# Performance work log

Hardware: AMD Instinct MI355X
Metric: run time of the kernel (lower is better)

The kernel has to match this reference:

```python
import jax, jax.numpy as jnp
import numpy as np

H = W = 32      # latent grid
WS = 8          # window size
NH = 8          # heads
C = 512         # channels
SHIFTS = (0, WS // 2)  # depth-2 Swin stage: W-MSA then SW-MSA


def _rel_pos_index(ws):
    coords = np.stack(np.meshgrid(np.arange(ws), np.arange(ws), indexing='ij'))
    flat = coords.reshape(2, -1)
    rel = (flat[:, :, None] - flat[:, None, :]).transpose(1, 2, 0).copy()
    rel[:, :, 0] += ws - 1
    rel[:, :, 1] += ws - 1
    rel[:, :, 0] *= 2 * ws - 1
    return jnp.asarray(rel.sum(-1))  # (ws*ws, ws*ws) int


def _attn_mask(h, w, ws, shift):
    img = np.zeros((h, w))
    cnt = 0
    sl = (slice(0, -ws), slice(-ws, -shift), slice(-shift, None))
    for hs in sl:
        for wsl in sl:
            img[hs, wsl] = cnt
            cnt += 1
    mw = img.reshape(h // ws, ws, w // ws, ws).transpose(0, 2, 1, 3).reshape(-1, ws * ws)
    m = mw[:, None, :] - mw[:, :, None]  # matches unsqueeze(1) - unsqueeze(2)
    return jnp.asarray(np.where(m != 0, -100.0, 0.0).astype(np.float32))  # (nW, N, N)


def _ln(x, g, b, eps=1e-5):
    mu = x.mean(-1, keepdims=True)
    var = ((x - mu) ** 2).mean(-1, keepdims=True)
    return (x - mu) * jax.lax.rsqrt(var + eps) * g + b


def _swin_block(x, shift, mask, rpi, n1g, n1b, qw, qb, rpb, pw, pb, n2g, n2b, f1w, f1b, f2w, f2b):
    B, L, Cc = x.shape
    N = WS * WS
    hd = Cc // NH
    shortcut = x
    h = _ln(x, n1g, n1b).reshape(B, H, W, Cc)
    if shift > 0:
        h = jnp.roll(h, (-shift, -shift), (1, 2))
    # window partition -> (B*nW, N, C)
    hw = h.reshape(B, H // WS, WS, W // WS, WS, Cc).transpose(0, 1, 3, 2, 4, 5).reshape(-1, N, Cc)
    qkv = (hw @ qw + qb).reshape(-1, N, 3, NH, hd).transpose(2, 0, 3, 1, 4)
    q, k, v = qkv[0], qkv[1], qkv[2]
    attn = jnp.einsum('bhnd,bhmd->bhnm', q * (hd ** -0.5), k)
    bias = rpb[rpi.reshape(-1)].reshape(N, N, NH).transpose(2, 0, 1)  # (NH, N, N)
    attn = attn + bias[None]
    if mask is not None:
        nW = mask.shape[0]
        attn = attn.reshape(-1, nW, NH, N, N) + mask[None, :, None]
        attn = attn.reshape(-1, NH, N, N)
    attn = jax.nn.softmax(attn, axis=-1)
    o = jnp.einsum('bhnm,bhmd->bhnd', attn, v).transpose(0, 2, 1, 3).reshape(-1, N, Cc)
    o = o @ pw + pb
    # window reverse
    o = o.reshape(B, H // WS, W // WS, WS, WS, Cc).transpose(0, 1, 3, 2, 4, 5).reshape(B, H, W, Cc)
    if shift > 0:
        o = jnp.roll(o, (shift, shift), (1, 2))
    x = shortcut + o.reshape(B, L, Cc)
    h2 = _ln(x, n2g, n2b)
    x = x + (jax.nn.gelu(h2 @ f1w + f1b, approximate=False) @ f2w + f2b)
    return x


def setup_inputs() -> dict:
    key = jax.random.key(0)
    ks = jax.random.split(key, 8)
    B, D, K = 32, 2, 4096
    s = 0.02
    return {
        'x': jax.random.normal(ks[0], (B, H * W, C), jnp.float32),
        'norm1_g': jnp.ones((D, C), jnp.float32),
        'norm1_b': jnp.zeros((D, C), jnp.float32),
        'qkv_w': jax.random.normal(ks[1], (D, C, 3 * C), jnp.float32) * s,
        'qkv_b': jnp.zeros((D, 3 * C), jnp.float32),
        'rpb_table': jax.random.normal(ks[2], (D, (2 * WS - 1) ** 2, NH), jnp.float32) * s,
        'proj_w': jax.random.normal(ks[3], (D, C, C), jnp.float32) * s,
        'proj_b': jnp.zeros((D, C), jnp.float32),
        'norm2_g': jnp.ones((D, C), jnp.float32),
        'norm2_b': jnp.zeros((D, C), jnp.float32),
        'fc1_w': jax.random.normal(ks[4], (D, C, 4 * C), jnp.float32) * s,
        'fc1_b': jnp.zeros((D, 4 * C), jnp.float32),
        'fc2_w': jax.random.normal(ks[5], (D, 4 * C, C), jnp.float32) * s,
        'fc2_b': jnp.zeros((D, C), jnp.float32),
        'codebook': jax.random.normal(ks[6], (K, C), jnp.float32),
    }


def reference(x, norm1_g, norm1_b, qkv_w, qkv_b, rpb_table, proj_w, proj_b,
              norm2_g, norm2_b, fc1_w, fc1_b, fc2_w, fc2_b, codebook):
    B, L, Cc = x.shape
    rpi = _rel_pos_index(WS)
    masks = [None, _attn_mask(H, W, WS, SHIFTS[1])]
    for i, shift in enumerate(SHIFTS):
        x = _swin_block(x, shift, masks[i], rpi,
                        norm1_g[i], norm1_b[i], qkv_w[i], qkv_b[i], rpb_table[i],
                        proj_w[i], proj_b[i], norm2_g[i], norm2_b[i],
                        fc1_w[i], fc1_b[i], fc2_w[i], fc2_b[i])
    # nearest-neighbor codebook quantization (cdist + argmin + gather)
    flat = x.reshape(-1, Cc)
    d = ((flat ** 2).sum(-1, keepdims=True)
         - 2.0 * flat @ codebook.T
         + (codebook ** 2).sum(-1))  # (B*L, K)
    idx = jnp.argmin(d, axis=-1)
    quant = codebook[idx]
    # straight-through estimator
    quant = flat + jax.lax.stop_gradient(quant - flat)
    return quant.reshape(B, L, Cc), idx.reshape(B, L)
```

## Files before the change

### kernel.cpp

```cpp
#include <hip/hip_runtime.h>
#include <math.h>

#define DEV __device__ __forceinline__

typedef __attribute__((ext_vector_type(8))) _Float16 f16x8;
typedef __attribute__((ext_vector_type(8))) short short8;
typedef __attribute__((ext_vector_type(4))) float f32x4;

namespace {

constexpr int C = 512;
constexpr int ROWS = 32768;
constexpr float LSCALE = 2048.0f;
constexpr float LINV   = 1.0f / 2048.0f;
constexpr float F16MIN = 6.1035156e-5f;

DEV void f2hsplit(float x, short& hs, short& ls) {
  _Float16 h = (_Float16)x;
  float hf = (float)h;
  if (fabsf(hf) < F16MIN) { h = (_Float16)0.0f; hf = 0.f; }
  _Float16 l = (_Float16)((x - hf) * LSCALE);
  if (fabsf((float)l) < F16MIN) l = (_Float16)0.0f;
  hs = __builtin_bit_cast(short, h);
  ls = __builtin_bit_cast(short, l);
}

DEV unsigned umn(unsigned a, unsigned b) { return a < b ? a : b; }
DEV unsigned umx(unsigned a, unsigned b) { return a > b ? a : b; }

DEV unsigned packkey(float d, int col) {
  unsigned u = __builtin_bit_cast(unsigned, d);
  u = (u & 0x80000000u) ? ~u : (u | 0x80000000u);
  return (u & 0xFFFFF000u) | (unsigned)col;
}
DEV float unpackd(unsigned k) {
  unsigned u = (k & 0x80000000u) ? (k ^ 0x80000000u) : ~k;
  return __builtin_bit_cast(float, u);
}

DEV int rowmap(int r, int shift) {
  int b  = r >> 10;
  int w  = (r >> 6) & 15;
  int wy = w >> 2, wx = w & 3;
  int ii = r & 63;
  int iy = ii >> 3, ix = ii & 7;
  int y = (wy * 8 + iy + shift) & 31;
  int x = (wx * 8 + ix + shift) & 31;
  return (b << 10) + (y << 5) + x;
}

DEV int region(int y) { return (y < 24) ? 0 : ((y < 28) ? 1 : 2); }

typedef __attribute__((address_space(1))) const unsigned int gu32;
typedef __attribute__((address_space(3))) unsigned int lu32;
DEV void gload16(const void* g, void* l) {
  __builtin_amdgcn_global_load_lds((gu32*)g, (lu32*)l, 16, 0, 0);
}

__global__ __launch_bounds__(256) void ln_split_kernel(
    const float* __restrict__ src, short* __restrict__ Hp, short* __restrict__ Lp,
    const float* __restrict__ g, const float* __restrict__ b,
    int shift, int windowed) {
  int wid  = (blockIdx.x * 256 + threadIdx.x) >> 6;
  int lane = threadIdx.x & 63;
  if (wid >= ROWS) return;
  int srcRow = windowed ? rowmap(wid, shift) : wid;
  const float* s = src + (size_t)srcRow * C + lane * 8;
  float v[8];
  *(float4*)(v)     = *(const float4*)(s);
  *(float4*)(v + 4) = *(const float4*)(s + 4);
  float sum = 0.f;
#pragma unroll
  for (int j = 0; j < 8; j++) sum += v[j];
#pragma unroll
  for (int o = 32; o >= 1; o >>= 1) sum += __shfl_xor(sum, o);
  float mu = sum * (1.0f / 512.0f);
  float vs = 0.f;
#pragma unroll
  for (int j = 0; j < 8; j++) { float d = v[j] - mu; vs += d * d; }
#pragma unroll
  for (int o = 32; o >= 1; o >>= 1) vs += __shfl_xor(vs, o);
  float rs = rsqrtf(vs * (1.0f / 512.0f) + 1e-5f);
  float gg[8], bb[8];
  *(float4*)gg       = *(const float4*)&g[lane * 8];
  *(float4*)(gg + 4) = *(const float4*)&g[lane * 8 + 4];
  *(float4*)bb       = *(const float4*)&b[lane * 8];
  *(float4*)(bb + 4) = *(const float4*)&b[lane * 8 + 4];
  short8 hv, lv;
#pragma unroll
  for (int j = 0; j < 8; j++) {
    float o8 = (v[j] - mu) * rs * gg[j] + bb[j];
    short hh, ll;
    f2hsplit(o8, hh, ll);
    hv[j] = hh; lv[j] = ll;
  }
  *(short8*)&Hp[(size_t)wid * C + lane * 8] = hv;
  *(short8*)&Lp[(size_t)wid * C + lane * 8] = lv;
}

__global__ __launch_bounds__(256) void rowss_kernel(
    const float* __restrict__ src, float* __restrict__ dst, int nrows) {
  int wid  = (blockIdx.x * 256 + threadIdx.x) >> 6;
  int lane = threadIdx.x & 63;
  if (wid >= nrows) return;
  const float* s = src + (size_t)wid * C + lane * 8;
  float4 a  = *(const float4*)s;
  float4 b4 = *(const float4*)(s + 4);
  float sum = a.x*a.x + a.y*a.y + a.z*a.z + a.w*a.w
            + b4.x*b4.x + b4.y*b4.y + b4.z*b4.z + b4.w*b4.w;
#pragma unroll
  for (int o = 32; o >= 1; o >>= 1) sum += __shfl_xor(sum, o);
  if (lane == 0) dst[wid] = sum;
}

__global__ __launch_bounds__(256) void wconvT_kernel(
    const float* __restrict__ W, short* __restrict__ Hp, short* __restrict__ Lp,
    int K, int N) {
  __shared__ float t[32][33];
  int tx = threadIdx.x, ty = threadIdx.y;
  int n0 = blockIdx.x * 32, k0 = blockIdx.y * 32;
#pragma unroll
  for (int r = 0; r < 4; r++) {
    int k = ty + r * 8;
    t[k][tx] = W[(size_t)(k0 + k) * N + n0 + tx];
  }
  __syncthreads();
#pragma unroll
  for (int r = 0; r < 4; r++) {
    int n = ty + r * 8;
    short h, l;
    f2hsplit(t[tx][n], h, l);
    Hp[(size_t)(n0 + n) * K + k0 + tx] = h;
    Lp[(size_t)(n0 + n) * K + k0 + tx] = l;
  }
}

__global__ __launch_bounds__(256) void wconv_kernel(
    const float* __restrict__ W, short* __restrict__ Hp, short* __restrict__ Lp) {
  size_t i = ((size_t)blockIdx.x * 256 + threadIdx.x) * 4;
  float4 a = *(const float4*)&W[i];
  float v[4] = {a.x, a.y, a.z, a.w};
  short hv[4], lv[4];
#pragma unroll
  for (int j = 0; j < 4; j++) f2hsplit(v[j], hv[j], lv[j]);
  *(short4*)&Hp[i] = *(short4*)hv;
  *(short4*)&Lp[i] = *(short4*)lv;
}

template <int EPI>
__global__ __launch_bounds__(512) void mgemm(
    const short* __restrict__ Ah, const short* __restrict__ Al,
    const short* __restrict__ Bh, const short* __restrict__ Bl,
    const int K, const float* __restrict__ bias,
    float* __restrict__ outF, short* __restrict__ outH, short* __restrict__ outL,
    const int ldo,
    const float* __restrict__ resid, const int rowOff, const int perm, const int shift) {
  __shared__ short lds[32768];
  const int m0 = blockIdx.x * 128, n0 = blockIdx.y * 128;
  const int t  = threadIdx.x;
  const int wv = t >> 6, ln = t & 63;
  const int wr = (wv >> 2) * 64, wc = (wv & 3) * 32;
  const int l15 = ln & 15, l4 = ln >> 4;

  f32x4 accH[4][2], accL[4][2];
#pragma unroll
  for (int mf = 0; mf < 4; mf++)
#pragma unroll
    for (int nf = 0; nf < 2; nf++) {
      accH[mf][nf] = (f32x4){0.f, 0.f, 0.f, 0.f};
      accL[mf][nf] = (f32x4){0.f, 0.f, 0.f, 0.f};
    }

  const int srow = ln >> 2;
  const int scol = ((ln & 3) ^ ((ln >> 3) & 3)) * 8;

  auto stage = [&](int buf, int k0) {
    short* b = lds + buf * 16384;
    size_t ra = (size_t)(m0 + wv * 16 + srow) * K + k0 + scol;
    size_t rb = (size_t)(n0 + wv * 16 + srow) * K + k0 + scol;
    gload16(Ah + ra, b + wv * 512);
    gload16(Bh + rb, b + 4096 + wv * 512);
    gload16(Al + ra, b + 8192 + wv * 512);
    gload16(Bl + rb, b + 12288 + wv * 512);
  };
  auto frag = [&](const short* lt, int rbase) -> f16x8 {
    int r = rbase + l15;
    int kc = l4 ^ ((r >> 1) & 3);
    return *(const f16x8*)(lt + (r >> 4) * 512 + (r & 15) * 32 + kc * 8);
  };

  stage(0, 0);
  __syncthreads();
  int cur = 0;
  for (int k0 = 0; k0 < K; k0 += 32) {
    if (k0 + 32 < K) stage(cur ^ 1, k0 + 32);
    const short* base = lds + cur * 16384;
    const short* As_h = base;
    const short* Bs_h = base + 4096;
    const short* As_l = base + 8192;
    const short* Bs_l = base + 12288;
    f16x8 ah[4], bh[2], bl[2];
#pragma unroll
    for (int mf = 0; mf < 4; mf++) ah[mf] = frag(As_h, wr + mf * 16);
#pragma unroll
    for (int nf = 0; nf < 2; nf++) bh[nf] = frag(Bs_h, wc + nf * 16);
#pragma unroll
    for (int mf = 0; mf < 4; mf++)
#pragma unroll
      for (int nf = 0; nf < 2; nf++)
        accH[mf][nf] = __builtin_amdgcn_mfma_f32_16x16x32_f16(ah[mf], bh[nf], accH[mf][nf], 0, 0, 0);
#pragma unroll
    for (int nf = 0; nf < 2; nf++) bl[nf] = frag(Bs_l, wc + nf * 16);
#pragma unroll
    for (int mf = 0; mf < 4; mf++)
#pragma unroll
      for (int nf = 0; nf < 2; nf++)
        accL[mf][nf] = __builtin_amdgcn_mfma_f32_16x16x32_f16(ah[mf], bl[nf], accL[mf][nf], 0, 0, 0);
#pragma unroll
    for (int mf = 0; mf < 4; mf++) {
      f16x8 al = frag(As_l, wr + mf * 16);
#pragma unroll
      for (int nf = 0; nf < 2; nf++)
        accL[mf][nf] = __builtin_amdgcn_mfma_f32_16x16x32_f16(al, bh[nf], accL[mf][nf], 0, 0, 0);
    }
    __syncthreads();
    cur ^= 1;
  }

  f32x4 acc[4][2];
#pragma unroll
  for (int mf = 0; mf < 4; mf++)
#pragma unroll
    for (int nf = 0; nf < 2; nf++)
#pragma unroll
      for (int r = 0; r < 4; r++)
        acc[mf][nf][r] = fmaf(accL[mf][nf][r], LINV, accH[mf][nf][r]);

  if (EPI == 0) {
#pragma unroll
    for (int mf = 0; mf < 4; mf++)
#pragma unroll
      for (int r = 0; r < 4; r++) {
        int row = m0 + wr + mf * 16 + l4 * 4 + r;
        float* op = outF + (size_t)row * ldo;
#pragma unroll
        for (int nf = 0; nf < 2; nf++) {
          int col = n0 + wc + nf * 16 + l15;
          op[col] = acc[mf][nf][r] + bias[col];
        }
      }
  } else if (EPI == 1) {
#pragma unroll
    for (int mf = 0; mf < 4; mf++)
#pragma unroll
      for (int r = 0; r < 4; r++) {
        int row = m0 + wr + mf * 16 + l4 * 4 + r;
#pragma unroll
        for (int nf = 0; nf < 2; nf++) {
          int col = n0 + wc + nf * 16 + l15;
          float v = acc[mf][nf][r] + bias[col];
          v = 0.5f * v * (1.0f + erff(v * 0.70710678118654752f));
          short h, l;
          f2hsplit(v, h, l);
          outH[(size_t)row * ldo + col] = h;
          outL[(size_t)row * ldo + col] = l;
        }
      }
  } else {
#pragma unroll
    for (int mf = 0; mf < 4; mf++)
#pragma unroll
      for (int r = 0; r < 4; r++) {
        int row = m0 + wr + mf * 16 + l4 * 4 + r;
        int orow = perm ? rowmap(row, shift) : (row + rowOff);
        const float* rp = resid + (size_t)orow * ldo;
        float* op = outF + (size_t)orow * ldo;
#pragma unroll
        for (int nf = 0; nf < 2; nf++) {
          int col = n0 + wc + nf * 16 + l15;
          float v = rp[col] + acc[mf][nf][r] + bias[col];
          op[col] = v;
          if (EPI == 4) {
            short h, l;
            f2hsplit(v, h, l);
            outH[(size_t)orow * ldo + col] = h;
            outL[(size_t)orow * ldo + col] = l;
          }
        }
      }
  }
}

__global__ __launch_bounds__(512) void vqgemm(
    const short* __restrict__ Ah, const short* __restrict__ Bh,
    const float* __restrict__ c2, unsigned* __restrict__ pk) {
  __shared__ short lds[16384];
  const int bid = blockIdx.x;
  const int xcd = bid & 7, idx = bid >> 3;
  const int m0 = (xcd * 32 + (idx & 31)) * 128;
  const int ny = idx >> 5;
  const int n0 = ny * 128;
  const int K = 512;
  const int t  = threadIdx.x;
  const int wv = t >> 6, ln = t & 63;
  const int wr = (wv >> 2) * 64, wc = (wv & 3) * 32;
  const int l15 = ln & 15, l4 = ln >> 4;

  f32x4 acc[4][2];
#pragma unroll
  for (int mf = 0; mf < 4; mf++)
#pragma unroll
    for (int nf = 0; nf < 2; nf++) acc[mf][nf] = (f32x4){0.f, 0.f, 0.f, 0.f};

  const int srow = ln >> 2;
  const int scol = ((ln & 3) ^ ((ln >> 3) & 3)) * 8;

  auto stage = [&](int buf, int k0) {
    short* b = lds + buf * 8192;
    size_t ra = (size_t)(m0 + wv * 16 + srow) * K + k0 + scol;
    size_t rb = (size_t)(n0 + wv * 16 + srow) * K + k0 + scol;
    gload16(Ah + ra, b + wv * 512);
    gload16(Bh + rb, b + 4096 + wv * 512);
  };
  auto frag = [&](const short* lt, int rbase) -> f16x8 {
    int r = rbase + l15;
    int kc = l4 ^ ((r >> 1) & 3);
    return *(const f16x8*)(lt + (r >> 4) * 512 + (r & 15) * 32 + kc * 8);
  };

  stage(0, 0);
  __syncthreads();
  int cur = 0;
  for (int k0 = 0; k0 < K; k0 += 32) {
    if (k0 + 32 < K) stage(cur ^ 1, k0 + 32);
    const short* base = lds + cur * 8192;
    f16x8 ah[4], bh[2];
#pragma unroll
    for (int mf = 0; mf < 4; mf++) ah[mf] = frag(base, wr + mf * 16);
#pragma unroll
    for (int nf = 0; nf < 2; nf++) bh[nf] = frag(base + 4096, wc + nf * 16);
#pragma unroll
    for (int mf = 0; mf < 4; mf++)
#pragma unroll
      for (int nf = 0; nf < 2; nf++)
        acc[mf][nf] = __builtin_amdgcn_mfma_f32_16x16x32_f16(ah[mf], bh[nf], acc[mf][nf], 0, 0, 0);
    __syncthreads();
    cur ^= 1;
  }

  unsigned* hk = (unsigned*)(void*)lds;
#pragma unroll
  for (int mf = 0; mf < 4; mf++)
#pragma unroll
    for (int r = 0; r < 4; r++) {
      int wrow = wr + mf * 16 + l4 * 4 + r;
      unsigned k1 = 0xFFFFFFFFu, k2 = 0xFFFFFFFFu;
#pragma unroll
      for (int nf = 0; nf < 2; nf++) {
        int col = n0 + wc + nf * 16 + l15;
        float d = c2[col] - 2.0f * acc[mf][nf][r];
        unsigned kk = packkey(d, col);
        if (kk < k1) { k2 = k1; k1 = kk; }
        else if (kk < k2) { k2 = kk; }
      }
#pragma unroll
      for (int o = 1; o <= 8; o <<= 1) {
        unsigned b1 = (unsigned)__shfl_xor((int)k1, o);
        unsigned b2 = (unsigned)__shfl_xor((int)k2, o);
        unsigned m1 = umn(k1, b1);
        unsigned m2 = umn(umx(k1, b1), umn(k2, b2));
        k1 = m1; k2 = m2;
      }
      if (l15 == 0) {
        hk[wrow * 8 + (wv & 3) * 2 + 0] = k1;
        hk[wrow * 8 + (wv & 3) * 2 + 1] = k2;
      }
    }
  __syncthreads();
  if (t < 128) {
    unsigned q1[4], q2[4];
#pragma unroll
    for (int i = 0; i < 4; i++) {
      q1[i] = hk[t * 8 + i * 2];
      q2[i] = hk[t * 8 + i * 2 + 1];
    }
    unsigned a1 = umn(q1[0], q1[1]);
    unsigned a2 = umn(umx(q1[0], q1[1]), umn(q2[0], q2[1]));
    unsigned b1 = umn(q1[2], q1[3]);
    unsigned b2 = umn(umx(q1[2], q1[3]), umn(q2[2], q2[3]));
    unsigned m1 = umn(a1, b1);
    unsigned m2 = umn(umx(a1, b1), umn(a2, b2));
    size_t base = (size_t)(m0 + t) * 64 + ny * 2;
    pk[base + 0] = m1;
    pk[base + 1] = m2;
  }
}

__global__ __launch_bounds__(256) void vq_out_kernel(
    const unsigned* __restrict__ pk, const float* __restrict__ x,
    const float* __restrict__ cb,
    float* __restrict__ outq, float* __restrict__ outidx) {
  int r = blockIdx.x * 4 + (threadIdx.x >> 6);
  int lane = threadIdx.x & 63;
  unsigned key = pk[(size_t)r * 64 + lane];
  unsigned kmin = key;
#pragma unroll
  for (int o = 32; o >= 1; o >>= 1) kmin = umn(kmin, (unsigned)__shfl_xor((int)kmin, o));
  float dmin = unpackd(kmin);
  unsigned long long mask = __ballot(unpackd(key) <= dmin + 2.0f);

  const float* xr = x + (size_t)r * C + lane * 8;
  float4 xa = *(const float4*)xr;
  float4 xb = *(const float4*)(xr + 4);

  float bestd = 3.4e38f;
  int   besti = 0x7fffffff;
  while (mask) {
    int l = __ffsll(mask) - 1;
    mask &= mask - 1;
    int col = ((unsigned)__shfl((int)key, l)) & 0xFFFu;
    const float* cr = cb + (size_t)col * C + lane * 8;
    float4 ca = *(const float4*)cr;
    float4 cb4 = *(const float4*)(cr + 4);
    float s = 0.f;
    s = fmaf(ca.x, ca.x - 2.f * xa.x, s);
    s = fmaf(ca.y, ca.y - 2.f * xa.y, s);
    s = fmaf(ca.z, ca.z - 2.f * xa.z, s);
    s = fmaf(ca.w, ca.w - 2.f * xa.w, s);
    s = fmaf(cb4.x, cb4.x - 2.f * xb.x, s);
    s = fmaf(cb4.y, cb4.y - 2.f * xb.y, s);
    s = fmaf(cb4.z, cb4.z - 2.f * xb.z, s);
    s = fmaf(cb4.w, cb4.w - 2.f * xb.w, s);
#pragma unroll
    for (int o = 32; o >= 1; o >>= 1) s += __shfl_xor(s, o);
    if (s < bestd || (s == bestd && col < besti)) { bestd = s; besti = col; }
  }
  const float4* src = (const float4*)(cb + (size_t)besti * C + lane * 8);
  float4*       dst = (float4*)(outq + (size_t)r * C + lane * 8);
  dst[0] = src[0];
  dst[1] = src[1];
  if (lane == 0) outidx[r] = (float)besti;
}

__global__ __launch_bounds__(256) void attn_kernel(
    const float* __restrict__ qkv,
    const float* __restrict__ rpb,
    short* __restrict__ Hout, short* __restrict__ Lout,
    int winOff, int shift) {
  int wl = blockIdx.x;
  int h  = blockIdx.y;
  int t  = threadIdx.x;
  __shared__ float q[64][64], k[64][64], v[64][64], pT[64][64];

  const float* base = qkv + (size_t)wl * 64 * 1536 + h * 64;
#pragma unroll
  for (int rep = 0; rep < 4; rep++) {
    int f = t + rep * 256;
    int i = f >> 4, dq = (f & 15) * 4;
    const float* rowp = base + (size_t)i * 1536 + dq;
    float4 qv = *(const float4*)(rowp);
    float4 kv = *(const float4*)(rowp + 512);
    float4 vv = *(const float4*)(rowp + 1024);
    q[i][dq] = qv.x * 0.125f; q[i][dq + 1] = qv.y * 0.125f;
    q[i][dq + 2] = qv.z * 0.125f; q[i][dq + 3] = qv.w * 0.125f;
    *(float4*)&k[i][dq] = kv;
    *(float4*)&v[i][dq] = vv;
  }
  __syncthreads();

  int i  = t >> 2;
  int jg = t & 3;
  int wim = (winOff + wl) & 15;
  int wy = wim >> 2, wx = wim & 3;
  int iy = i >> 3, ix = i & 7;

  float qreg[64];
#pragma unroll
  for (int d = 0; d < 64; d += 4) *(float4*)&qreg[d] = *(float4*)&q[i][d];

  int ci = 0;
  if (shift) ci = region(wy * 8 + iy) * 3 + region(wx * 8 + ix);

  float sc[16];
#pragma unroll
  for (int jj = 0; jj < 16; jj++) {
    int j = jg * 16 + jj;
    float s = 0.f;
#pragma unroll
    for (int d = 0; d < 64; d += 4) {
      float4 kv = *(float4*)&k[j][d];
      s = fmaf(qreg[d], kv.x, s);
      s = fmaf(qreg[d + 1], kv.y, s);
      s = fmaf(qreg[d + 2], kv.z, s);
      s = fmaf(qreg[d + 3], kv.w, s);
    }
    int jy = j >> 3, jx = j & 7;
    s += rpb[((iy - jy + 7) * 15 + (ix - jx + 7)) * 8 + h];
    if (shift) {
      int cj = region(wy * 8 + jy) * 3 + region(wx * 8 + jx);
      if (ci != cj) s -= 100.0f;
    }
    sc[jj] = s;
  }
  float mx = sc[0];
#pragma unroll
  for (int jj = 1; jj < 16; jj++) mx = fmaxf(mx, sc[jj]);
  mx = fmaxf(mx, __shfl_xor(mx, 1));
  mx = fmaxf(mx, __shfl_xor(mx, 2));
  float sum = 0.f;
#pragma unroll
  for (int jj = 0; jj < 16; jj++) { sc[jj] = expf(sc[jj] - mx); sum += sc[jj]; }
  sum += __shfl_xor(sum, 1);
  sum += __shfl_xor(sum, 2);
  float inv = 1.0f / sum;
#pragma unroll
  for (int jj = 0; jj < 16; jj++) pT[jg * 16 + jj][i] = sc[jj] * inv;
  __syncthreads();

  float accv[16];
#pragma unroll
  for (int dd = 0; dd < 16; dd++) accv[dd] = 0.f;
  for (int j = 0; j < 64; j++) {
    float pij = pT[j][i];
#pragma unroll
    for (int dd = 0; dd < 16; dd += 4) {
      float4 vv = *(float4*)&v[j][jg * 16 + dd];
      accv[dd]     = fmaf(pij, vv.x, accv[dd]);
      accv[dd + 1] = fmaf(pij, vv.y, accv[dd + 1]);
      accv[dd + 2] = fmaf(pij, vv.z, accv[dd + 2]);
      accv[dd + 3] = fmaf(pij, vv.w, accv[dd + 3]);
    }
  }
  size_t obase = ((size_t)(winOff + wl) * 64 + i) * 512 + h * 64 + jg * 16;
  short8 hv, lv;
#pragma unroll
  for (int half = 0; half < 2; half++) {
#pragma unroll
    for (int j = 0; j < 8; j++) {
      short hh, ll;
      f2hsplit(accv[half * 8 + j], hh, ll);
      hv[j] = hh; lv[j] = ll;
    }
    *(short8*)&Hout[obase + half * 8] = hv;
    *(short8*)&Lout[obase + half * 8] = lv;
  }
}

}

extern "C" void kernel_launch(void* const* d_in, const int* in_sizes, int n_in,
                              void* d_out, int out_size, void* d_ws, size_t ws_size,
                              hipStream_t stream) {
  const float* x_in = (const float*)d_in[0];
  const float* n1g  = (const float*)d_in[1];
  const float* n1b  = (const float*)d_in[2];
  const float* qkvw = (const float*)d_in[3];
  const float* qkvb = (const float*)d_in[4];
  const float* rpb  = (const float*)d_in[5];
  const float* pw   = (const float*)d_in[6];
  const float* pb   = (const float*)d_in[7];
  const float* n2g  = (const float*)d_in[8];
  const float* n2b  = (const float*)d_in[9];
  const float* f1w  = (const float*)d_in[10];
  const float* f1b  = (const float*)d_in[11];
  const float* f2w  = (const float*)d_in[12];
  const float* f2b_ = (const float*)d_in[13];
  const float* cb   = (const float*)d_in[14];

  float* outq   = (float*)d_out;
  float* outidx = outq + 16777216;
  short* Hbuf = (short*)d_out;
  short* Lbuf = Hbuf + (size_t)ROWS * 512;

  char* ws = (char*)d_ws;
  float* Abuf = (float*)ws;
  short* Wb   = (short*)(ws + ((size_t)64 << 20));
  char*  Cbuf = ws + ((size_t)96 << 20);
  const int Rrows = (ws_size >= ((size_t)232 << 20)) ? 16384
                  : (ws_size >= ((size_t)160 << 20)) ? 8192
                  : (ws_size >= ((size_t)128 << 20)) ? 4096 : 2048;

  const int SZ_QKV = 512 * 1536, SZ_P = 512 * 512, SZ_F1 = 512 * 2048, SZ_F2 = 2048 * 512;
  const int PB = (SZ_QKV + SZ_P + SZ_F1 + SZ_F2) * 2;
  short* cbH = Wb + (size_t)2 * PB;
  short* cbL = cbH + 4096 * 512;

  for (int blk = 0; blk < 2; blk++) {
    short* base = Wb + (size_t)blk * PB;
    short* qH = base;          short* qL = qH + SZ_QKV;
    short* pH = qL + SZ_QKV;   short* pL = pH + SZ_P;
    short* f1H = pL + SZ_P;    short* f1L = f1H + SZ_F1;
    short* f2H = f1L + SZ_F1;  short* f2L = f2H + SZ_F2;
    wconvT_kernel<<<dim3(48, 16), dim3(32, 8), 0, stream>>>(qkvw + (size_t)blk * SZ_QKV, qH, qL, 512, 1536);
    wconvT_kernel<<<dim3(16, 16), dim3(32, 8), 0, stream>>>(pw + (size_t)blk * SZ_P, pH, pL, 512, 512);
    wconvT_kernel<<<dim3(64, 16), dim3(32, 8), 0, stream>>>(f1w + (size_t)blk * SZ_F1, f1H, f1L, 512, 2048);
    wconvT_kernel<<<dim3(16, 64), dim3(32, 8), 0, stream>>>(f2w + (size_t)blk * SZ_F2, f2H, f2L, 2048, 512);
  }
  wconv_kernel<<<2048, 256, 0, stream>>>(cb, cbH, cbL);

  const int nch = ROWS / Rrows;
  for (int blk = 0; blk < 2; blk++) {
    short* base = Wb + (size_t)blk * PB;
    short* qH = base;          short* qL = qH + SZ_QKV;
    short* pH = qL + SZ_QKV;   short* pL = pH + SZ_P;
    short* f1H = pL + SZ_P;    short* f1L = f1H + SZ_F1;
    short* f2H = f1L + SZ_F1;  short* f2L = f2H + SZ_F2;
    const float* xcur = blk ? (const float*)Abuf : x_in;
    int shift = blk ? 4 : 0;

    ln_split_kernel<<<8192, 256, 0, stream>>>(xcur, Hbuf, Lbuf, n1g + blk * 512, n1b + blk * 512, shift, 1);

    float* Cq = (float*)Cbuf;
    for (int ch = 0; ch < nch; ch++) {
      int r0 = ch * Rrows;
      mgemm<0><<<dim3(Rrows / 128, 12), 512, 0, stream>>>(
          Hbuf + (size_t)r0 * 512, Lbuf + (size_t)r0 * 512, qH, qL, 512,
          qkvb + blk * 1536, Cq, nullptr, nullptr, 1536,
          nullptr, 0, 0, 0);
      attn_kernel<<<dim3(Rrows / 64, 8), 256, 0, stream>>>(
          Cq, rpb + blk * 1800, Hbuf, Lbuf, r0 >> 6, shift);
    }

    mgemm<2><<<dim3(256, 4), 512, 0, stream>>>(
        Hbuf, Lbuf, pH, pL, 512, pb + blk * 512,
        Abuf, nullptr, nullptr, 512,
        blk ? (const float*)Abuf : x_in, 0, 1, shift);

    ln_split_kernel<<<8192, 256, 0, stream>>>(Abuf, Hbuf, Lbuf, n2g + blk * 512, n2b + blk * 512, 0, 0);

    short* gh = (short*)Cbuf;
    short* gl = gh + (size_t)Rrows * 2048;
    for (int ch = 0; ch < nch; ch++) {
      int r0 = ch * Rrows;
      mgemm<1><<<dim3(Rrows / 128, 16), 512, 0, stream>>>(
          Hbuf + (size_t)r0 * 512, Lbuf + (size_t)r0 * 512, f1H, f1L, 512,
          f1b + blk * 2048, nullptr, gh, gl, 2048,
          nullptr, 0, 0, 0);
      if (blk == 0) {
        mgemm<2><<<dim3(Rrows / 128, 4), 512, 0, stream>>>(
            gh, gl, f2H, f2L, 2048, f2b_ + blk * 512,
            Abuf, nullptr, nullptr, 512,
            Abuf, r0, 0, 0);
      } else {
        mgemm<4><<<dim3(Rrows / 128, 4), 512, 0, stream>>>(
            gh, gl, f2H, f2L, 2048, f2b_ + blk * 512,
            Abuf, Hbuf, Lbuf, 512,
            Abuf, r0, 0, 0);
      }
    }
  }

  float*    c2  = (float*)Cbuf;
  unsigned* pkb = (unsigned*)(Cbuf + ((size_t)64 << 10));
  rowss_kernel<<<1024, 256, 0, stream>>>(cb, c2, 4096);
  vqgemm<<<8192, 512, 0, stream>>>(Hbuf, cbH, c2, pkb);
  vq_out_kernel<<<8192, 256, 0, stream>>>(pkb, Abuf, cb, outq, outidx);
}
```

Measured before the change: 2.343 ms.

## Widen VQ GEMM tile to 256 codes and drop LDS double buffering

The codebook-distance GEMM now covers 256 codebook columns per block instead of 128. That halves the grid and the number of A-tile reloads, and each wave computes a 64x64 sub-tile with 16 accumulators. The double-buffered prefetch is replaced by a single LDS buffer loaded by three staging slots per wave, with a sync before and after compute. The partial-key buffer shrinks to 32 candidates per row, and the output kernel masks the upper lanes. The tradeoff is less global-load/compute overlap and more registers per thread, in exchange for more reuse of each A tile.

Measured after the change: 2.331 ms. Within noise of the previous version (-0.5%).

```diff
diff --git a/kernel.cpp b/kernel.cpp
--- a/kernel.cpp
+++ b/kernel.cpp
@@ -294,58 +294,60 @@
 __global__ __launch_bounds__(512) void vqgemm(
     const short* __restrict__ Ah, const short* __restrict__ Bh,
     const float* __restrict__ c2, unsigned* __restrict__ pk) {
-  __shared__ short lds[16384];
+  __shared__ short lds[12288];
   const int bid = blockIdx.x;
   const int xcd = bid & 7, idx = bid >> 3;
   const int m0 = (xcd * 32 + (idx & 31)) * 128;
   const int ny = idx >> 5;
-  const int n0 = ny * 128;
+  const int n0 = ny * 256;
   const int K = 512;
   const int t  = threadIdx.x;
   const int wv = t >> 6, ln = t & 63;
-  const int wr = (wv >> 2) * 64, wc = (wv & 3) * 32;
+  const int wr = (wv >> 2) * 64, wc = (wv & 3) * 64;
   const int l15 = ln & 15, l4 = ln >> 4;
 
-  f32x4 acc[4][2];
+  f32x4 acc[4][4];
 #pragma unroll
   for (int mf = 0; mf < 4; mf++)
 #pragma unroll
-    for (int nf = 0; nf < 2; nf++) acc[mf][nf] = (f32x4){0.f, 0.f, 0.f, 0.f};
+    for (int nf = 0; nf < 4; nf++) acc[mf][nf] = (f32x4){0.f, 0.f, 0.f, 0.f};
 
   const int srow = ln >> 2;
   const int scol = ((ln & 3) ^ ((ln >> 3) & 3)) * 8;
 
-  auto stage = [&](int buf, int k0) {
-    short* b = lds + buf * 8192;
-    size_t ra = (size_t)(m0 + wv * 16 + srow) * K + k0 + scol;
-    size_t rb = (size_t)(n0 + wv * 16 + srow) * K + k0 + scol;
-    gload16(Ah + ra, b + wv * 512);
-    gload16(Bh + rb, b + 4096 + wv * 512);
-  };
+  short* As = lds;
+  short* Bs = lds + 4096;
+
   auto frag = [&](const short* lt, int rbase) -> f16x8 {
     int r = rbase + l15;
     int kc = l4 ^ ((r >> 1) & 3);
     return *(const f16x8*)(lt + (r >> 4) * 512 + (r & 15) * 32 + kc * 8);
   };
 
-  stage(0, 0);
-  __syncthreads();
-  int cur = 0;
   for (int k0 = 0; k0 < K; k0 += 32) {
-    if (k0 + 32 < K) stage(cur ^ 1, k0 + 32);
-    const short* base = lds + cur * 8192;
-    f16x8 ah[4], bh[2];
-#pragma unroll
-    for (int mf = 0; mf < 4; mf++) ah[mf] = frag(base, wr + mf * 16);
-#pragma unroll
-    for (int nf = 0; nf < 2; nf++) bh[nf] = frag(base + 4096, wc + nf * 16);
+#pragma unroll
+    for (int q = 0; q < 3; q++) {
+      int s = wv * 3 + q;
+      int isA = (s < 8);
+      int c = isA ? s : (s - 8);
+      const short* src = isA ? Ah : Bh;
+      short* dst = (isA ? As : Bs) + c * 512;
+      int rowbase = (isA ? m0 : n0) + c * 16;
+      size_t ga = (size_t)(rowbase + srow) * K + k0 + scol;
+      gload16(src + ga, dst);
+    }
+    __syncthreads();
+    f16x8 ah[4], bh[4];
+#pragma unroll
+    for (int mf = 0; mf < 4; mf++) ah[mf] = frag(As, wr + mf * 16);
+#pragma unroll
+    for (int nf = 0; nf < 4; nf++) bh[nf] = frag(Bs, wc + nf * 16);
 #pragma unroll
     for (int mf = 0; mf < 4; mf++)
 #pragma unroll
-      for (int nf = 0; nf < 2; nf++)
+      for (int nf = 0; nf < 4; nf++)
         acc[mf][nf] = __builtin_amdgcn_mfma_f32_16x16x32_f16(ah[mf], bh[nf], acc[mf][nf], 0, 0, 0);
     __syncthreads();
-    cur ^= 1;
   }
 
   unsigned* hk = (unsigned*)(void*)lds;
@@ -356,7 +358,7 @@
       int wrow = wr + mf * 16 + l4 * 4 + r;
       unsigned k1 = 0xFFFFFFFFu, k2 = 0xFFFFFFFFu;
 #pragma unroll
-      for (int nf = 0; nf < 2; nf++) {
+      for (int nf = 0; nf < 4; nf++) {
         int col = n0 + wc + nf * 16 + l15;
         float d = c2[col] - 2.0f * acc[mf][nf][r];
         unsigned kk = packkey(d, col);
@@ -390,7 +392,7 @@
     unsigned b2 = umn(umx(q1[2], q1[3]), umn(q2[2], q2[3]));
     unsigned m1 = umn(a1, b1);
     unsigned m2 = umn(umx(a1, b1), umn(a2, b2));
-    size_t base = (size_t)(m0 + t) * 64 + ny * 2;
+    size_t base = (size_t)(m0 + t) * 32 + ny * 2;
     pk[base + 0] = m1;
     pk[base + 1] = m2;
   }
@@ -402,12 +404,12 @@
     float* __restrict__ outq, float* __restrict__ outidx) {
   int r = blockIdx.x * 4 + (threadIdx.x >> 6);
   int lane = threadIdx.x & 63;
-  unsigned key = pk[(size_t)r * 64 + lane];
+  unsigned key = (lane < 32) ? pk[(size_t)r * 32 + lane] : 0xFFFFFFFFu;
   unsigned kmin = key;
 #pragma unroll
   for (int o = 32; o >= 1; o >>= 1) kmin = umn(kmin, (unsigned)__shfl_xor((int)kmin, o));
   float dmin = unpackd(kmin);
-  unsigned long long mask = __ballot(unpackd(key) <= dmin + 2.0f);
+  unsigned long long mask = __ballot(lane < 32 && unpackd(key) <= dmin + 2.0f);
 
   const float* xr = x + (size_t)r * C + lane * 8;
   float4 xa = *(const float4*)xr;
@@ -653,6 +655,6 @@
   float*    c2  = (float*)Cbuf;
   unsigned* pkb = (unsigned*)(Cbuf + ((size_t)64 << 10));
   rowss_kernel<<<1024, 256, 0, stream>>>(cb, c2, 4096);
-  vqgemm<<<8192, 512, 0, stream>>>(Hbuf, cbH, c2, pkb);
+  vqgemm<<<4096, 512, 0, stream>>>(Hbuf, cbH, c2, pkb);
   vq_out_kernel<<<8192, 256, 0, stream>>>(pkb, Abuf, cb, outq, outidx);
 }
```
